# Kernel optimization log

Measured on AMD Instinct MI355X. Metric: run time of the kernel, lower is better.

The kernel has to match this reference:

```python
import jax, jax.numpy as jnp
import numpy as np

N_NODES = 100000
N_EDGES = 600000
N_FEAT = 166
HID = 128


def _ln(x, g, b, eps=1e-5):
    m = x.mean(-1, keepdims=True)
    v = ((x - m) ** 2).mean(-1, keepdims=True)
    return (x - m) * jax.lax.rsqrt(v + eps) * g + b


def _gcn(h, row, col, em, W, b, n):
    # PyG GCNConv with add_self_loops=True; em is a 0/1 edge mask (recent/history split)
    hl = h @ W.T  # [N,H], PyG internal Linear has no bias
    deg = jax.ops.segment_sum(em, col, num_segments=n) + 1.0  # +1 for self loop
    dis = jax.lax.rsqrt(deg)
    coef = em * dis[row] * dis[col]
    agg = jax.ops.segment_sum(hl[row] * coef[:, None], col, num_segments=n)
    agg = agg + hl * (dis * dis)[:, None]  # self-loop message
    return agg + b


def setup_inputs():
    key = jax.random.key(0)
    ks = jax.random.split(key, 16)
    f32 = jnp.float32
    H = HID
    z = lambda *s: jnp.zeros(s, f32)
    nrm = lambda k, s, sc=0.05: jax.random.normal(k, s, f32) * sc
    return {
        "x": jax.random.normal(ks[0], (N_NODES, N_FEAT), f32),
        "edge_index": jax.random.randint(ks[1], (2, N_EDGES), 0, N_NODES, jnp.int32),
        "timestamps": jax.random.uniform(ks[2], (N_EDGES,), f32),
        "memory": nrm(ks[3], (N_NODES, H), 0.1),
        "W_in": nrm(ks[4], (H, N_FEAT)), "b_in": z(H),
        "W_time": nrm(ks[5], (H, 1)), "b_time": z(H),
        "W_ih": nrm(ks[6], (3 * H, H)), "W_hh": nrm(ks[7], (3 * H, H)),
        "b_ih": z(3 * H), "b_hh": z(3 * H),
        "W_gr": nrm(ks[8], (H, H)), "b_gr": z(H),
        "W_gh": nrm(ks[9], (H, H)), "b_gh": z(H),
        "ln_pa_g": jnp.ones((H,), f32), "ln_pa_b": z(H),
        "Wv": nrm(ks[10], (H, H)), "bv": z(H),
        "Wo": nrm(ks[11], (H, H)), "bo": z(H),
        "ln_at_g": jnp.ones((H,), f32), "ln_at_b": z(H),
        "W1": nrm(ks[12], (64, H)), "b1": z(64),
        "W2": nrm(ks[13], (2, 64)), "b2": z(2),
    }


def reference(x, edge_index, timestamps, memory, W_in, b_in, W_time, b_time,
              W_ih, W_hh, b_ih, b_hh, W_gr, b_gr, W_gh, b_gh,
              ln_pa_g, ln_pa_b, Wv, bv, Wo, bo, ln_at_g, ln_at_b,
              W1, b1, W2, b2):
    n = x.shape[0]
    row, col = edge_index[0], edge_index[1]
    # input projection + scatter-max temporal encoding
    h = x @ W_in.T + b_in
    nt = jnp.maximum(jax.ops.segment_max(timestamps, col, num_segments=n), 0.0)  # torch_scatter max inits at 0
    tmin, tmax = nt.min(), nt.max()
    nt = jnp.where(tmax > tmin, (nt - tmin) / (tmax - tmin + 1e-8), nt)
    h = h + nt[:, None] * W_time[:, 0] + b_time  # Linear(1, H)
    h = jax.nn.relu(h)
    h = h + memory
    # gather -> GRUCell -> scatter memory update for nodes touched by any edge
    upd = jnp.zeros((n,), bool).at[edge_index.reshape(-1)].set(True)
    gi = h @ W_ih.T + b_ih
    gh = memory @ W_hh.T + b_hh
    ir, iz, ic = jnp.split(gi, 3, axis=1)
    hr, hz, hc = jnp.split(gh, 3, axis=1)
    r = jax.nn.sigmoid(ir + hr)
    z = jax.nn.sigmoid(iz + hz)
    c = jnp.tanh(ic + r * hc)
    new_memory = jnp.where(upd[:, None], (1.0 - z) * c + z * memory, memory)
    # split edges by median timestamp, two GCN paths
    med = jnp.median(timestamps)
    m_rec = (timestamps >= med).astype(h.dtype)
    h_rec = _gcn(h, row, col, m_rec, W_gr, b_gr, n)
    h_his = _gcn(h, row, col, 1.0 - m_rec, W_gh, b_gh, n)
    # multi-path aggregation with softmax over per-path mean scores
    stacked = jnp.stack([h_rec, h_his], axis=1)  # [N,2,H]
    w = jax.nn.softmax(stacked.mean(-1), axis=-1)[..., None]
    h = _ln((stacked * w).sum(1), ln_pa_g, ln_pa_b)
    # anomaly attention: L=S=1 per "batch" element, so softmax over one key == 1
    # => attended = out_proj(v_proj(x)); query path cancels exactly
    attended = (h @ Wv.T + bv) @ Wo.T + bo
    h = _ln(h + attended, ln_at_g, ln_at_b)
    # classifier (eval mode: dropout = identity)
    logits = jax.nn.relu(h @ W1.T + b1) @ W2.T + b2
    return logits, new_memory
```

## Files before the change

### kernel.cpp

```cpp
#include <hip/hip_runtime.h>

#define NN 100000
#define NE 600000
#define NF 166
#define NH 128
#define NNH 12800000

enum { EPI_PLAIN = 0, EPI_RELU = 2, EPI_H = 3, EPI_HEAD = 4 };

typedef short bf16x8 __attribute__((ext_vector_type(8)));
typedef float f32x16 __attribute__((ext_vector_type(16)));

__device__ __forceinline__ unsigned short f2bf(float f) {
  unsigned u = __float_as_uint(f);
  u += 0x7fffu + ((u >> 16) & 1u);
  return (unsigned short)(u >> 16);
}

__device__ __forceinline__ void gl_lds16(const void* g, void* l) {
  __builtin_amdgcn_global_load_lds((__attribute__((address_space(1))) void*)(void*)g,
                                   (__attribute__((address_space(3))) void*)l, 16, 0, 0);
}

template<int EPI, bool WF32, bool WB16, bool BIAS2, bool CONC, bool DUALA, int NT>
__launch_bounds__(256)
__global__ void mgemm(const unsigned short* __restrict__ A, int lda,
                      const unsigned short* __restrict__ A2,
                      const unsigned short* __restrict__ W, int ldw,
                      float* __restrict__ C, int ldc,
                      unsigned short* __restrict__ Cb, int ldcb,
                      int K, int M,
                      const float* __restrict__ bias, const float* __restrict__ bias2,
                      const float* __restrict__ wtv, const float* __restrict__ ntv,
                      const float* __restrict__ mem, const int* __restrict__ scal)
{
  __shared__ unsigned short As[128 * 64];
  __shared__ unsigned short Bs[128 * 64];
  const int tid = threadIdx.x;
  const int wave = tid >> 6, lane = tid & 63;
  const int row0 = blockIdx.y * 128, col0 = blockIdx.x * 128;
  if (DUALA && blockIdx.x) { A = A2; bias = bias2; }
  const int hi = lane >> 5, l5 = lane & 31, l3 = lane & 7;
  f32x16 acc[NT] = {};

  for (int k0 = 0; k0 < K; k0 += 64) {
    const unsigned short* Asrc = A;
    int kk = k0;
    if (CONC && k0 >= 128) { Asrc = A2; kk = k0 - 128; }
    __syncthreads();
#pragma unroll
    for (int q = 0; q < 4; ++q) {
      int id = q * 256 + tid;
      int r = id >> 3, cch = id & 7;
      int sw = ((cch ^ (r & 7)) << 3);
      int gr = row0 + r; if (gr > NN - 1) gr = NN - 1;
      gl_lds16(Asrc + (size_t)gr * lda + kk + sw, &As[(q * 256 + wave * 64) * 8]);
      if (q < NT) {
        int gm = col0 + r; if (gm > M - 1) gm = M - 1;
        gl_lds16(W + (size_t)gm * ldw + k0 + sw, &Bs[(q * 256 + wave * 64) * 8]);
      }
    }
    __syncthreads();
#pragma unroll
    for (int s = 0; s < 4; ++s) {
      int slot8 = (((s * 2 + hi) ^ l3) << 3);
      bf16x8 a = *(const bf16x8*)&As[(wave * 32 + l5) * 64 + slot8];
#pragma unroll
      for (int t = 0; t < NT; ++t) {
        bf16x8 b = *(const bf16x8*)&Bs[(t * 32 + l5) * 64 + slot8];
        acc[t] = __builtin_amdgcn_mfma_f32_32x32x16_bf16(a, b, acc[t], 0, 0, 0);
      }
    }
  }

  float tmin = 0.f, tmax = 0.f;
  if (EPI == EPI_H) { tmin = __int_as_float(scal[5]); tmax = __int_as_float(scal[6]); }
  float bc[NT], wc[NT];
#pragma unroll
  for (int t = 0; t < NT; ++t) {
    int gcol = col0 + t * 32 + l5;
    int bcol = DUALA ? (gcol & 127) : gcol;
    bc[t] = bias ? bias[bcol] : 0.f;
    if (BIAS2) bc[t] += bias2[gcol];
    if (EPI == EPI_H) { bc[t] += bias2[gcol]; wc[t] = wtv[gcol]; }
  }
#pragma unroll
  for (int rg = 0; rg < 16; ++rg) {
    int lr = (rg & 3) + 8 * (rg >> 2) + 4 * hi;
    int grow = row0 + wave * 32 + lr;
    if (grow >= NN) continue;
    float ntn = 0.f;
    if (EPI == EPI_H) {
      ntn = ntv[grow];
      if (tmax > tmin) ntn = (ntn - tmin) / (tmax - tmin + 1e-8f);
    }
    float hv[NT];
#pragma unroll
    for (int t = 0; t < NT; ++t) {
      float v = acc[t][rg] + bc[t];
      if (EPI == EPI_RELU || EPI == EPI_HEAD) v = fmaxf(v, 0.f);
      if (EPI == EPI_H) {
        v += ntn * wc[t];
        v = fmaxf(v, 0.f);
        v += mem[(size_t)grow * NH + (col0 + t * 32 + l5)];
      }
      hv[t] = v;
    }
    if (EPI == EPI_HEAD) {
      float p0 = hv[0] * wtv[l5]      + hv[1] * wtv[32 + l5];
      float p1 = hv[0] * wtv[64 + l5] + hv[1] * wtv[96 + l5];
#pragma unroll
      for (int d = 1; d < 32; d <<= 1) { p0 += __shfl_xor(p0, d); p1 += __shfl_xor(p1, d); }
      if (l5 == 0) {
        C[(size_t)grow * 2]     = p0 + bias2[0];
        C[(size_t)grow * 2 + 1] = p1 + bias2[1];
      }
    } else {
#pragma unroll
      for (int t = 0; t < NT; ++t) {
        int gcol = col0 + t * 32 + l5;
        if (WF32) C[(size_t)grow * ldc + gcol] = hv[t];
        if (WB16) Cb[(size_t)grow * ldcb + gcol] = f2bf(hv[t]);
      }
    }
  }
}

__global__ void conv_x(const float* __restrict__ x, unsigned short* __restrict__ xb)
{
  int i = blockIdx.x * 256 + threadIdx.x;
  if (i >= NN * 192) return;
  int n = i / 192, c = i - n * 192;
  xb[i] = (c < NF) ? f2bf(x[n * NF + c]) : (unsigned short)0;
}

__global__ void conv_mem(const float* __restrict__ m, unsigned short* __restrict__ mb)
{
  int i = blockIdx.x * 256 + threadIdx.x;
  if (i >= NNH) return;
  mb[i] = f2bf(m[i]);
}

__global__ void conv_w(const float* __restrict__ Wi, const float* __restrict__ Wih,
                       const float* __restrict__ Whh, const float* __restrict__ Wgr,
                       const float* __restrict__ Wgh, const float* __restrict__ Wv,
                       const float* __restrict__ Wo, const float* __restrict__ W1,
                       unsigned short* __restrict__ wb)
{
  int i = blockIdx.x * 256 + threadIdx.x;
  if (i >= 196608) return;
  float v;
  if (i < 24576)       { int r = i / 192, c = i - r * 192; v = (c < NF) ? Wi[r * NF + c] : 0.f; }
  else if (i < 90112)  { int j = i - 24576; int r = j >> 8, c = j & 255;
                         v = (c < 128) ? Wih[r * 128 + c] : Whh[r * 128 + (c - 128)]; }
  else if (i < 122880) { int j = i - 90112; int r = j >> 7, c = j & 127;
                         v = (r < 128) ? Wih[(256 + r) * 128 + c] : Whh[(128 + r) * 128 + c]; }
  else if (i < 139264) v = Wgr[i - 122880];
  else if (i < 155648) v = Wgh[i - 139264];
  else if (i < 172032) v = Wv[i - 155648];
  else if (i < 188416) v = Wo[i - 172032];
  else                 v = W1[i - 188416];
  wb[i] = f2bf(v);
}

__global__ void compose_att(const float* __restrict__ Wv, const float* __restrict__ Wo,
                            const float* __restrict__ bv, const float* __restrict__ bo,
                            unsigned short* __restrict__ wout, float* __restrict__ bout)
{
  int i = blockIdx.x * 256 + threadIdx.x;
  if (i >= 16384) return;
  int r = i >> 7, c = i & 127;
  float s = 0.f;
  for (int k = 0; k < 128; ++k) s = fmaf(Wo[r * 128 + k], Wv[k * 128 + c], s);
  wout[i] = f2bf(s);
  if (c == 0) {
    float t = bo[r];
    for (int k = 0; k < 128; ++k) t = fmaf(Wo[r * 128 + k], bv[k], t);
    bout[r] = t;
  }
}

__device__ __forceinline__ int ts_bin(float t) {
  int b = (int)(t * 65536.0f);
  return b > 65535 ? 65535 : (b < 0 ? 0 : b);
}

__global__ void edge_pass1(const int* __restrict__ row, const int* __restrict__ col,
                           const float* __restrict__ ts,
                           float* nt, int* upd, int* cnt_all, int* hist1)
{
  int e = blockIdx.x * 256 + threadIdx.x;
  if (e >= NE) return;
  int r = row[e], c = col[e];
  float t = ts[e];
  atomicMax((int*)(nt + c), __float_as_int(t));
  upd[r] = 1; upd[c] = 1;
  atomicAdd(cnt_all + c, 1);
  atomicAdd(hist1 + ts_bin(t), 1);
}

__global__ void node_minmax(const float* __restrict__ nt, int* scal)
{
  int i = blockIdx.x * 256 + threadIdx.x;
  float v = (i < NN) ? nt[i] : nt[0];
  float vmin = v, vmax = v;
#pragma unroll
  for (int d = 1; d < 64; d <<= 1) {
    vmin = fminf(vmin, __shfl_xor(vmin, d));
    vmax = fmaxf(vmax, __shfl_xor(vmax, d));
  }
  __shared__ float smin[4], smax[4];
  int lane = threadIdx.x & 63, w = threadIdx.x >> 6;
  if (lane == 0) { smin[w] = vmin; smax[w] = vmax; }
  __syncthreads();
  if (threadIdx.x == 0) {
    float a = fminf(fminf(smin[0], smin[1]), fminf(smin[2], smin[3]));
    float b = fmaxf(fmaxf(smax[0], smax[1]), fmaxf(smax[2], smax[3]));
    atomicMin(scal + 5, __float_as_int(a));
    atomicMax(scal + 6, __float_as_int(b));
  }
}

__global__ void scan_hist1(const int* __restrict__ hist, int* scal)
{
  const int K1 = 299999, K2 = 300000;
  __shared__ int sums[256];
  __shared__ int pre[257];
  int t = threadIdx.x;
  int s = 0;
  for (int i = 0; i < 256; ++i) s += hist[t * 256 + i];
  sums[t] = s;
  __syncthreads();
  if (t == 0) { int run = 0; for (int i = 0; i < 256; ++i) { pre[i] = run; run += sums[i]; } pre[256] = run; }
  __syncthreads();
  int base = pre[t], nexts = base + sums[t];
  if (K1 >= base && K1 < nexts) {
    int run = base;
    for (int i = 0; i < 256; ++i) {
      int cv = hist[t * 256 + i];
      if (K1 < run + cv) { scal[0] = t * 256 + i; scal[1] = run; break; }
      run += cv;
    }
  }
  if (K2 >= base && K2 < nexts) {
    int run = base;
    for (int i = 0; i < 256; ++i) {
      int cv = hist[t * 256 + i];
      if (K2 < run + cv) { scal[2] = t * 256 + i; scal[3] = run; break; }
      run += cv;
    }
  }
}

#define CAND_CAP 4096
__global__ void collect_cand(const float* __restrict__ ts, const int* __restrict__ scal,
                             float* cand1, float* cand2, int* ccnt)
{
  int e = blockIdx.x * 256 + threadIdx.x;
  if (e >= NE) return;
  float t = ts[e];
  int b = ts_bin(t);
  if (b == scal[0]) {
    int s = atomicAdd(ccnt + 0, 1);
    if (s < CAND_CAP) cand1[s] = t;
  }
  if (b == scal[2]) {
    int s = atomicAdd(ccnt + 1, 1);
    if (s < CAND_CAP) cand2[s] = t;
  }
}

__global__ void select_med(const float* __restrict__ c1, const float* __restrict__ c2,
                           const int* __restrict__ ccnt, int* scal)
{
  __shared__ float res[2];
  for (int which = 0; which < 2; ++which) {
    const float* c = which ? c2 : c1;
    int m = ccnt[which]; if (m > CAND_CAP) m = CAND_CAP;
    int rank = which ? (300000 - scal[3]) : (299999 - scal[1]);
    for (int i = threadIdx.x; i < m; i += 256) {
      float v = c[i];
      int less = 0, eq = 0;
      for (int j = 0; j < m; ++j) { float w = c[j]; less += (w < v); eq += (w == v); }
      if (less <= rank && rank < less + eq) res[which] = v;
    }
  }
  __syncthreads();
  if (threadIdx.x == 0)
    ((float*)scal)[4] = 0.5f * (res[0] + res[1]);
}

__global__ void csr_scan1(const int* __restrict__ cnt, int* loc, int* bsum)
{
  __shared__ int s[256];
  int t = threadIdx.x;
  int i = blockIdx.x * 256 + t;
  int v = (i < NN) ? cnt[i] : 0;
  s[t] = v;
  __syncthreads();
  for (int d = 1; d < 256; d <<= 1) {
    int add = (t >= d) ? s[t - d] : 0;
    __syncthreads();
    s[t] += add;
    __syncthreads();
  }
  if (i < NN) loc[i] = s[t] - v;
  if (t == 255) bsum[blockIdx.x] = s[255];
}

__global__ void csr_scan2(int* bsum, int nb)
{
  if (threadIdx.x == 0) {
    int run = 0;
    for (int i = 0; i < nb; ++i) { int v = bsum[i]; bsum[i] = run; run += v; }
  }
}

__global__ void csr_scan3(const int* __restrict__ loc, const int* __restrict__ bsum,
                          int* off, int* fillpos)
{
  int i = blockIdx.x * 256 + threadIdx.x;
  if (i < NN) {
    int o = loc[i] + bsum[i >> 8];
    off[i] = o;
    fillpos[i] = o;
  }
  if (i == 0) off[NN] = NE;
}

__global__ void csr_fill(const int* __restrict__ row, const int* __restrict__ col,
                         const float* __restrict__ ts, const int* __restrict__ scal,
                         int* fillpos, int* elist, int* cnt_rec)
{
  int e = blockIdx.x * 256 + threadIdx.x;
  if (e >= NE) return;
  int c = col[e], r = row[e];
  int rec = (ts[e] >= __int_as_float(scal[4])) ? 1 : 0;
  if (rec) atomicAdd(cnt_rec + c, 1);
  int slot = atomicAdd(fillpos + c, 1);
  elist[slot] = r | (rec << 31);
}

__global__ void node_dis(const int* __restrict__ cnt_all, const int* __restrict__ cnt_rec,
                         float* dr, float* dh)
{
  int n = blockIdx.x * 256 + threadIdx.x;
  if (n >= NN) return;
  int ca = cnt_all[n], cr = cnt_rec[n];
  dr[n] = rsqrtf((float)cr + 1.f);
  dh[n] = rsqrtf((float)(ca - cr) + 1.f);
}

__device__ __forceinline__ float gru1(float rp, float zp, float ic, float hc, float mv) {
  float r = 1.f / (1.f + expf(-rp));
  float z = 1.f / (1.f + expf(-zp));
  float c = tanhf(ic + r * hc);
  return (1.f - z) * c + z * mv;
}

__global__ void gru_kernel(const float* __restrict__ RZ, const float* __restrict__ ICHC,
                           const float* __restrict__ mem, const int* __restrict__ upd,
                           float* __restrict__ out)
{
  int idx = blockIdx.x * 256 + threadIdx.x;
  if (idx >= NN * 32) return;
  int n = idx >> 5, q = (idx & 31) << 2;
  size_t p128 = (size_t)n * 128 + q;
  size_t p256 = (size_t)n * 256 + q;
  float4 mv = *(const float4*)(mem + p128);
  float4 o = mv;
  if (upd[n]) {
    float4 rp = *(const float4*)(RZ + p256);
    float4 zp = *(const float4*)(RZ + p256 + 128);
    float4 ic = *(const float4*)(ICHC + p256);
    float4 hc = *(const float4*)(ICHC + p256 + 128);
    o.x = gru1(rp.x, zp.x, ic.x, hc.x, mv.x);
    o.y = gru1(rp.y, zp.y, ic.y, hc.y, mv.y);
    o.z = gru1(rp.z, zp.z, ic.z, hc.z, mv.z);
    o.w = gru1(rp.w, zp.w, ic.w, hc.w, mv.w);
  }
  *(float4*)(out + p128) = o;
}

__global__ void gather_combine(const int* __restrict__ off, const int* __restrict__ elist,
                               const float* __restrict__ dis_r, const float* __restrict__ dis_h,
                               const float* __restrict__ hl2,
                               const float* __restrict__ bgr, const float* __restrict__ bgh,
                               const float* __restrict__ g, const float* __restrict__ b,
                               float* h2f, unsigned short* h2b)
{
  int n = blockIdx.x * 4 + (threadIdx.x >> 6);
  if (n >= NN) return;
  int lane = threadIdx.x & 63;
  int o0 = off[n], o1 = off[n + 1];
  float dnr = dis_r[n], dnh = dis_h[n];
  float arx = 0.f, ary = 0.f, ahx = 0.f, ahy = 0.f;
  int j = o0;
  for (; j + 1 < o1; j += 2) {
    int p0 = elist[j], p1 = elist[j + 1];
    int r0 = p0 & 0x7fffffff, r1 = p1 & 0x7fffffff;
    int c0 = ((unsigned)p0) >> 31, c1 = ((unsigned)p1) >> 31;
    float d0 = c0 ? dis_r[r0] : dis_h[r0];
    float d1 = c1 ? dis_r[r1] : dis_h[r1];
    const float2 v0 = *(const float2*)(hl2 + (size_t)r0 * 256 + ((c0 ^ 1) << 7) + (lane << 1));
    const float2 v1 = *(const float2*)(hl2 + (size_t)r1 * 256 + ((c1 ^ 1) << 7) + (lane << 1));
    float k0 = d0 * (c0 ? dnr : dnh);
    float k1 = d1 * (c1 ? dnr : dnh);
    if (c0) { arx = fmaf(k0, v0.x, arx); ary = fmaf(k0, v0.y, ary); }
    else    { ahx = fmaf(k0, v0.x, ahx); ahy = fmaf(k0, v0.y, ahy); }
    if (c1) { arx = fmaf(k1, v1.x, arx); ary = fmaf(k1, v1.y, ary); }
    else    { ahx = fmaf(k1, v1.x, ahx); ahy = fmaf(k1, v1.y, ahy); }
  }
  if (j < o1) {
    int p0 = elist[j];
    int r0 = p0 & 0x7fffffff;
    int c0 = ((unsigned)p0) >> 31;
    float d0 = c0 ? dis_r[r0] : dis_h[r0];
    const float2 v0 = *(const float2*)(hl2 + (size_t)r0 * 256 + ((c0 ^ 1) << 7) + (lane << 1));
    float k0 = d0 * (c0 ? dnr : dnh);
    if (c0) { arx = fmaf(k0, v0.x, arx); ary = fmaf(k0, v0.y, ary); }
    else    { ahx = fmaf(k0, v0.x, ahx); ahy = fmaf(k0, v0.y, ahy); }
  }
  const float2 lr = *(const float2*)(hl2 + (size_t)n * 256 + (lane << 1));
  const float2 lh = *(const float2*)(hl2 + (size_t)n * 256 + 128 + (lane << 1));
  float2 br = *(const float2*)(bgr + (lane << 1));
  float2 bh = *(const float2*)(bgh + (lane << 1));
  float rx = arx + lr.x * dnr * dnr + br.x;
  float ry = ary + lr.y * dnr * dnr + br.y;
  float hx = ahx + lh.x * dnh * dnh + bh.x;
  float hy = ahy + lh.y * dnh * dnh + bh.y;
  float sa = rx + ry, sc = hx + hy;
#pragma unroll
  for (int d = 1; d < 64; d <<= 1) { sa += __shfl_xor(sa, d); sc += __shfl_xor(sc, d); }
  float m0 = sa * (1.f / 128.f), m1 = sc * (1.f / 128.f);
  float mx = fmaxf(m0, m1);
  float e0 = expf(m0 - mx), e1 = expf(m1 - mx);
  float inv = 1.f / (e0 + e1);
  float w0 = e0 * inv, w1 = e1 * inv;
  float yx = w0 * rx + w1 * hx;
  float yy = w0 * ry + w1 * hy;
  float s = yx + yy;
#pragma unroll
  for (int d = 1; d < 64; d <<= 1) s += __shfl_xor(s, d);
  float mean = s * (1.f / 128.f);
  float dx = yx - mean, dy = yy - mean;
  float vv = dx * dx + dy * dy;
#pragma unroll
  for (int d = 1; d < 64; d <<= 1) vv += __shfl_xor(vv, d);
  float rstd = rsqrtf(vv * (1.f / 128.f) + 1e-5f);
  float2 gg = *(const float2*)(g + (lane << 1));
  float2 bb = *(const float2*)(b + (lane << 1));
  float ox = dx * rstd * gg.x + bb.x;
  float oy = dy * rstd * gg.y + bb.y;
  int offo = n * NH + (lane << 1);
  *(float2*)(h2f + offo) = make_float2(ox, oy);
  *(unsigned*)(h2b + offo) = (unsigned)f2bf(ox) | ((unsigned)f2bf(oy) << 16);
}

__global__ void ln_residual(const float* __restrict__ x, const float* __restrict__ y,
                            const float* __restrict__ g, const float* __restrict__ b,
                            unsigned short* out)
{
  int n = blockIdx.x * 4 + (threadIdx.x >> 6);
  if (n >= NN) return;
  int lane = threadIdx.x & 63;
  int off = n * NH + (lane << 1);
  float2 xv = *(const float2*)(x + off);
  float2 yv = *(const float2*)(y + off);
  float ax = xv.x + yv.x, ay = xv.y + yv.y;
  float s = ax + ay;
#pragma unroll
  for (int d = 1; d < 64; d <<= 1) s += __shfl_xor(s, d);
  float mean = s * (1.f / 128.f);
  float dx = ax - mean, dy = ay - mean;
  float vv = dx * dx + dy * dy;
#pragma unroll
  for (int d = 1; d < 64; d <<= 1) vv += __shfl_xor(vv, d);
  float rstd = rsqrtf(vv * (1.f / 128.f) + 1e-5f);
  float2 gg = *(const float2*)(g + (lane << 1));
  float2 bb = *(const float2*)(b + (lane << 1));
  float ox = dx * rstd * gg.x + bb.x;
  float oy = dy * rstd * gg.y + bb.y;
  *(unsigned*)(out + off) = (unsigned)f2bf(ox) | ((unsigned)f2bf(oy) << 16);
}

extern "C" void kernel_launch(void* const* d_in, const int* in_sizes, int n_in,
                              void* d_out, int out_size, void* d_ws, size_t ws_size,
                              hipStream_t stream)
{
  const float* x      = (const float*)d_in[0];
  const int*   ei     = (const int*)  d_in[1];
  const float* ts     = (const float*)d_in[2];
  const float* mem    = (const float*)d_in[3];
  const float* W_in   = (const float*)d_in[4];
  const float* b_in   = (const float*)d_in[5];
  const float* W_time = (const float*)d_in[6];
  const float* b_time = (const float*)d_in[7];
  const float* W_ih   = (const float*)d_in[8];
  const float* W_hh   = (const float*)d_in[9];
  const float* b_ih   = (const float*)d_in[10];
  const float* b_hh   = (const float*)d_in[11];
  const float* W_gr   = (const float*)d_in[12];
  const float* b_gr   = (const float*)d_in[13];
  const float* W_gh   = (const float*)d_in[14];
  const float* b_gh   = (const float*)d_in[15];
  const float* ln_pa_g= (const float*)d_in[16];
  const float* ln_pa_b= (const float*)d_in[17];
  const float* Wv     = (const float*)d_in[18];
  const float* bv     = (const float*)d_in[19];
  const float* Wo     = (const float*)d_in[20];
  const float* bo     = (const float*)d_in[21];
  const float* ln_at_g= (const float*)d_in[22];
  const float* ln_at_b= (const float*)d_in[23];
  const float* W1     = (const float*)d_in[24];
  const float* b1     = (const float*)d_in[25];
  const float* W2     = (const float*)d_in[26];
  const float* b2     = (const float*)d_in[27];

  const int* row = ei;
  const int* col = ei + NE;
  float* out_logits = (float*)d_out;
  float* out_mem    = (float*)d_out + NN * 2;

  float* ws = (float*)d_ws;
  unsigned short* hb  = (unsigned short*)(ws);
  float* rz           = ws + 6400000;
  unsigned short* xb  = (unsigned short*)(ws + 6400000);
  int* hist1          = (int*)(ws + 16000000);
  float* ichc         = ws + 32000000;
  unsigned short* memb= (unsigned short*)(ws + 57600000);
  unsigned short* wb  = (unsigned short*)(ws + 64000000);
  float* nt           = ws + 64100000;
  float* dis_r        = ws + 64200000;
  float* dis_h        = ws + 64300000;
  int* cnt_all        = (int*)(ws + 64400000);
  int* cnt_rec        = (int*)(ws + 64500000);
  int* upd            = (int*)(ws + 64600000);
  int* scal           = (int*)(ws + 64700000);
  float* batt         = ws + 64705000;
  float* cand1        = ws + 64710000;
  float* cand2        = ws + 64715000;
  int* ccnt           = (int*)(ws + 64720000);
  float* h2f   = ws + 6400000;
  int* off     = (int*)(ws + 19200000);
  int* fillpos = (int*)(ws + 19350000);
  int* loc     = (int*)(ws + 19500000);
  int* bsum    = (int*)(ws + 19700000);
  int* elist   = (int*)(ws + 19800000);
  float* hl2   = ws + 32000000;
  unsigned short* h2bb = hb;
  float* att           = ws + 32000000;
  unsigned short* rb   = (unsigned short*)(ws + 44800000);

  unsigned short* wb_in = wb;
  unsigned short* wb_rz = wb + 24576;
  unsigned short* wb_c  = wb + 90112;
  unsigned short* wb_gr = wb + 122880;
  unsigned short* wb_v  = wb + 155648;
  unsigned short* wb_o  = wb + 172032;
  unsigned short* wb_1  = wb + 188416;

  hipMemsetAsync(nt,      0, NN * 4, stream);
  hipMemsetAsync(cnt_all, 0, NN * 4, stream);
  hipMemsetAsync(cnt_rec, 0, NN * 4, stream);
  hipMemsetAsync(upd,     0, NN * 4, stream);
  hipMemsetAsync(hist1,   0, 65536 * 4, stream);
  hipMemsetAsync(scal,    0, 16 * 4, stream);
  hipMemsetAsync(scal + 5,0x7f, 4, stream);
  hipMemsetAsync(ccnt,    0, 8, stream);

  const int eb  = (NE + 255) / 256;
  const int nb  = (NN + 255) / 256;
  dim3 blk(256);

  edge_pass1  <<<eb, 256, 0, stream>>>(row, col, ts, nt, upd, cnt_all, hist1);
  node_minmax <<<nb, 256, 0, stream>>>(nt, scal);
  scan_hist1  <<<1, 256, 0, stream>>>(hist1, scal);
  collect_cand<<<eb, 256, 0, stream>>>(ts, scal, cand1, cand2, ccnt);
  select_med  <<<1, 256, 0, stream>>>(cand1, cand2, ccnt, scal);

  conv_w     <<<768, 256, 0, stream>>>(W_in, W_ih, W_hh, W_gr, W_gh, Wv, Wo, W1, wb);
  compose_att<<<64, 256, 0, stream>>>(Wv, Wo, bv, bo, wb_o, batt);
  conv_x     <<<75000, 256, 0, stream>>>(x, xb);
  conv_mem   <<<50000, 256, 0, stream>>>(mem, memb);

  auto gg = [](int M) { return dim3((unsigned)((M + 127) / 128), (NN + 127) / 128); };

  mgemm<EPI_H, false, true, false, false, false, 4><<<gg(128), blk, 0, stream>>>(
      xb, 192, nullptr, wb_in, 192, nullptr, 0, hb, NH, 192, 128,
      b_in, b_time, W_time, nt, mem, scal);
  mgemm<EPI_PLAIN, true, false, true, true, false, 4><<<gg(256), blk, 0, stream>>>(
      hb, NH, memb, wb_rz, 256, rz, 256, nullptr, 0, 256, 256,
      b_ih, b_hh, nullptr, nullptr, nullptr, nullptr);
  mgemm<EPI_PLAIN, true, false, false, false, true, 4><<<gg(256), blk, 0, stream>>>(
      hb, NH, memb, wb_c, NH, ichc, 256, nullptr, 0, 128, 256,
      b_ih + 256, b_hh + 256, nullptr, nullptr, nullptr, nullptr);
  gru_kernel<<<(NN * 32) / 256, 256, 0, stream>>>(rz, ichc, mem, upd, out_mem);

  csr_scan1<<<nb, 256, 0, stream>>>(cnt_all, loc, bsum);
  csr_scan2<<<1, 64, 0, stream>>>(bsum, nb);
  csr_scan3<<<nb, 256, 0, stream>>>(loc, bsum, off, fillpos);
  csr_fill <<<eb, 256, 0, stream>>>(row, col, ts, scal, fillpos, elist, cnt_rec);
  node_dis <<<nb, 256, 0, stream>>>(cnt_all, cnt_rec, dis_r, dis_h);

  mgemm<EPI_PLAIN, true, false, false, false, false, 4><<<gg(256), blk, 0, stream>>>(
      hb, NH, nullptr, wb_gr, NH, hl2, 256, nullptr, 0, 128, 256,
      nullptr, nullptr, nullptr, nullptr, nullptr, nullptr);

  gather_combine<<<(NN + 3) / 4, 256, 0, stream>>>(off, elist, dis_r, dis_h, hl2,
      b_gr, b_gh, ln_pa_g, ln_pa_b, h2f, h2bb);

  mgemm<EPI_PLAIN, true, false, false, false, false, 4><<<gg(128), blk, 0, stream>>>(
      h2bb, NH, nullptr, wb_o, NH, att, NH, nullptr, 0, 128, 128,
      batt, nullptr, nullptr, nullptr, nullptr, nullptr);
  ln_residual<<<(NN + 3) / 4, 256, 0, stream>>>(h2f, att, ln_at_g, ln_at_b, rb);

  mgemm<EPI_HEAD, false, false, false, false, false, 2><<<gg(64), blk, 0, stream>>>(
      rb, NH, nullptr, wb_1, NH, out_logits, 0, nullptr, 0, 128, 64,
      b1, b2, W2, nullptr, nullptr, nullptr);

  (void)in_sizes; (void)n_in; (void)out_size; (void)ws_size;
}
```

Baseline: 811.7 us.

## Fuse LN into attention GEMM, drop conv_mem, and store intermediates in fp16

The attention output projection now runs LayerNorm and the residual add in its epilogue, which removes the separate ln_residual kernel and the fp32 att and h2f round trips. The input-projection GEMM writes the bf16 copy of memory as a side output, so the conv_mem pass is gone. GRU pre-activations, GCN linear outputs and h2 are stored as fp16 rather than fp32, which halves gather and GRU traffic. Wider N tiles (NT=8) let one block cover all 256 output columns. The attention GEMM now uses the fp16 MFMA, and the change accepts fp16 rounding on these intermediates.

Result: faster. 758.2 us (-6.6%).

```diff
diff --git a/kernel.cpp b/kernel.cpp
--- a/kernel.cpp
+++ b/kernel.cpp
@@ -6,10 +6,13 @@
 #define NH 128
 #define NNH 12800000
 
-enum { EPI_PLAIN = 0, EPI_RELU = 2, EPI_H = 3, EPI_HEAD = 4 };
+enum { EPI_PLAIN = 0, EPI_RELU = 2, EPI_H = 3, EPI_HEAD = 4, EPI_ATTLN = 5 };
 
 typedef short bf16x8 __attribute__((ext_vector_type(8)));
 typedef float f32x16 __attribute__((ext_vector_type(16)));
+typedef _Float16 f16x2 __attribute__((ext_vector_type(2)));
+typedef _Float16 f16x4 __attribute__((ext_vector_type(4)));
+typedef _Float16 f16x8 __attribute__((ext_vector_type(8)));
 
 __device__ __forceinline__ unsigned short f2bf(float f) {
   unsigned u = __float_as_uint(f);
@@ -17,12 +20,16 @@
   return (unsigned short)(u >> 16);
 }
 
+__device__ __forceinline__ unsigned short f2h(float f) {
+  return __builtin_bit_cast(unsigned short, (_Float16)f);
+}
+
 __device__ __forceinline__ void gl_lds16(const void* g, void* l) {
   __builtin_amdgcn_global_load_lds((__attribute__((address_space(1))) void*)(void*)g,
                                    (__attribute__((address_space(3))) void*)l, 16, 0, 0);
 }
 
-template<int EPI, bool WF32, bool WB16, bool BIAS2, bool CONC, bool DUALA, int NT>
+template<int EPI, int OUTK, bool BIAS2, bool CONC, bool DUALA, bool F16, int NT>
 __launch_bounds__(256)
 __global__ void mgemm(const unsigned short* __restrict__ A, int lda,
                       const unsigned short* __restrict__ A2,
@@ -35,10 +42,10 @@
                       const float* __restrict__ mem, const int* __restrict__ scal)
 {
   __shared__ unsigned short As[128 * 64];
-  __shared__ unsigned short Bs[128 * 64];
+  __shared__ unsigned short Bs[NT * 32 * 64];
   const int tid = threadIdx.x;
   const int wave = tid >> 6, lane = tid & 63;
-  const int row0 = blockIdx.y * 128, col0 = blockIdx.x * 128;
+  const int row0 = blockIdx.y * 128, col0 = blockIdx.x * NT * 32;
   if (DUALA && blockIdx.x) { A = A2; bias = bias2; }
   const int hi = lane >> 5, l5 = lane & 31, l3 = lane & 7;
   f32x16 acc[NT] = {};
@@ -55,10 +62,14 @@
       int sw = ((cch ^ (r & 7)) << 3);
       int gr = row0 + r; if (gr > NN - 1) gr = NN - 1;
       gl_lds16(Asrc + (size_t)gr * lda + kk + sw, &As[(q * 256 + wave * 64) * 8]);
-      if (q < NT) {
-        int gm = col0 + r; if (gm > M - 1) gm = M - 1;
-        gl_lds16(W + (size_t)gm * ldw + k0 + sw, &Bs[(q * 256 + wave * 64) * 8]);
-      }
+    }
+#pragma unroll
+    for (int q = 0; q < NT; ++q) {
+      int id = q * 256 + tid;
+      int r = id >> 3, cch = id & 7;
+      int sw = ((cch ^ (r & 7)) << 3);
+      int gm = col0 + r; if (gm > M - 1) gm = M - 1;
+      gl_lds16(W + (size_t)gm * ldw + k0 + sw, &Bs[(q * 256 + wave * 64) * 8]);
     }
     __syncthreads();
 #pragma unroll
@@ -68,21 +79,26 @@
 #pragma unroll
       for (int t = 0; t < NT; ++t) {
         bf16x8 b = *(const bf16x8*)&Bs[(t * 32 + l5) * 64 + slot8];
-        acc[t] = __builtin_amdgcn_mfma_f32_32x32x16_bf16(a, b, acc[t], 0, 0, 0);
+        if (F16)
+          acc[t] = __builtin_amdgcn_mfma_f32_32x32x16_f16(
+              __builtin_bit_cast(f16x8, a), __builtin_bit_cast(f16x8, b), acc[t], 0, 0, 0);
+        else
+          acc[t] = __builtin_amdgcn_mfma_f32_32x32x16_bf16(a, b, acc[t], 0, 0, 0);
       }
     }
   }
 
   float tmin = 0.f, tmax = 0.f;
   if (EPI == EPI_H) { tmin = __int_as_float(scal[5]); tmax = __int_as_float(scal[6]); }
-  float bc[NT], wc[NT];
+  float bc[NT], wc[NT], b2c[NT];
 #pragma unroll
   for (int t = 0; t < NT; ++t) {
     int gcol = col0 + t * 32 + l5;
     int bcol = DUALA ? (gcol & 127) : gcol;
     bc[t] = bias ? bias[bcol] : 0.f;
     if (BIAS2) bc[t] += bias2[gcol];
-    if (EPI == EPI_H) { bc[t] += bias2[gcol]; wc[t] = wtv[gcol]; }
+    if (EPI == EPI_H)     { bc[t] += bias2[gcol]; wc[t] = wtv[gcol]; }
+    if (EPI == EPI_ATTLN) { wc[t] = wtv[gcol]; b2c[t] = bias2[gcol]; }
   }
 #pragma unroll
   for (int rg = 0; rg < 16; ++rg) {
@@ -102,9 +118,31 @@
       if (EPI == EPI_H) {
         v += ntn * wc[t];
         v = fmaxf(v, 0.f);
-        v += mem[(size_t)grow * NH + (col0 + t * 32 + l5)];
+        float mv = mem[(size_t)grow * NH + (col0 + t * 32 + l5)];
+        v += mv;
+        ((unsigned short*)C)[(size_t)grow * NH + (col0 + t * 32 + l5)] = f2bf(mv);
       }
       hv[t] = v;
+    }
+    if (EPI == EPI_ATTLN) {
+      const _Float16* h2r = (const _Float16*)mem;
+      float s = 0.f;
+#pragma unroll
+      for (int t = 0; t < NT; ++t) {
+        hv[t] += (float)h2r[(size_t)grow * NH + (col0 + t * 32 + l5)];
+        s += hv[t];
+      }
+#pragma unroll
+      for (int d = 1; d < 32; d <<= 1) s += __shfl_xor(s, d);
+      float mean = s * (1.f / 128.f);
+      float var = 0.f;
+#pragma unroll
+      for (int t = 0; t < NT; ++t) { hv[t] -= mean; var += hv[t] * hv[t]; }
+#pragma unroll
+      for (int d = 1; d < 32; d <<= 1) var += __shfl_xor(var, d);
+      float rstd = rsqrtf(var * (1.f / 128.f) + 1e-5f);
+#pragma unroll
+      for (int t = 0; t < NT; ++t) hv[t] = hv[t] * rstd * wc[t] + b2c[t];
     }
     if (EPI == EPI_HEAD) {
       float p0 = hv[0] * wtv[l5]      + hv[1] * wtv[32 + l5];
@@ -119,8 +157,9 @@
 #pragma unroll
       for (int t = 0; t < NT; ++t) {
         int gcol = col0 + t * 32 + l5;
-        if (WF32) C[(size_t)grow * ldc + gcol] = hv[t];
-        if (WB16) Cb[(size_t)grow * ldcb + gcol] = f2bf(hv[t]);
+        if (OUTK == 1) C[(size_t)grow * ldc + gcol] = hv[t];
+        if (OUTK == 2) Cb[(size_t)grow * ldcb + gcol] = f2bf(hv[t]);
+        if (OUTK == 3) Cb[(size_t)grow * ldcb + gcol] = f2h(hv[t]);
       }
     }
   }
@@ -132,13 +171,6 @@
   if (i >= NN * 192) return;
   int n = i / 192, c = i - n * 192;
   xb[i] = (c < NF) ? f2bf(x[n * NF + c]) : (unsigned short)0;
-}
-
-__global__ void conv_mem(const float* __restrict__ m, unsigned short* __restrict__ mb)
-{
-  int i = blockIdx.x * 256 + threadIdx.x;
-  if (i >= NNH) return;
-  mb[i] = f2bf(m[i]);
 }
 
 __global__ void conv_w(const float* __restrict__ Wi, const float* __restrict__ Wih,
@@ -165,14 +197,14 @@
 
 __global__ void compose_att(const float* __restrict__ Wv, const float* __restrict__ Wo,
                             const float* __restrict__ bv, const float* __restrict__ bo,
-                            unsigned short* __restrict__ wout, float* __restrict__ bout)
+                            _Float16* __restrict__ wout, float* __restrict__ bout)
 {
   int i = blockIdx.x * 256 + threadIdx.x;
   if (i >= 16384) return;
   int r = i >> 7, c = i & 127;
   float s = 0.f;
   for (int k = 0; k < 128; ++k) s = fmaf(Wo[r * 128 + k], Wv[k * 128 + c], s);
-  wout[i] = f2bf(s);
+  wout[i] = (_Float16)s;
   if (c == 0) {
     float t = bo[r];
     for (int k = 0; k < 128; ++k) t = fmaf(Wo[r * 128 + k], bv[k], t);
@@ -358,7 +390,7 @@
   return (1.f - z) * c + z * mv;
 }
 
-__global__ void gru_kernel(const float* __restrict__ RZ, const float* __restrict__ ICHC,
+__global__ void gru_kernel(const _Float16* __restrict__ RZ, const _Float16* __restrict__ ICHC,
                            const float* __restrict__ mem, const int* __restrict__ upd,
                            float* __restrict__ out)
 {
@@ -370,65 +402,67 @@
   float4 mv = *(const float4*)(mem + p128);
   float4 o = mv;
   if (upd[n]) {
-    float4 rp = *(const float4*)(RZ + p256);
-    float4 zp = *(const float4*)(RZ + p256 + 128);
-    float4 ic = *(const float4*)(ICHC + p256);
-    float4 hc = *(const float4*)(ICHC + p256 + 128);
-    o.x = gru1(rp.x, zp.x, ic.x, hc.x, mv.x);
-    o.y = gru1(rp.y, zp.y, ic.y, hc.y, mv.y);
-    o.z = gru1(rp.z, zp.z, ic.z, hc.z, mv.z);
-    o.w = gru1(rp.w, zp.w, ic.w, hc.w, mv.w);
+    f16x4 rp = *(const f16x4*)(RZ + p256);
+    f16x4 zp = *(const f16x4*)(RZ + p256 + 128);
+    f16x4 ic = *(const f16x4*)(ICHC + p256);
+    f16x4 hc = *(const f16x4*)(ICHC + p256 + 128);
+    o.x = gru1((float)rp[0], (float)zp[0], (float)ic[0], (float)hc[0], mv.x);
+    o.y = gru1((float)rp[1], (float)zp[1], (float)ic[1], (float)hc[1], mv.y);
+    o.z = gru1((float)rp[2], (float)zp[2], (float)ic[2], (float)hc[2], mv.z);
+    o.w = gru1((float)rp[3], (float)zp[3], (float)ic[3], (float)hc[3], mv.w);
   }
   *(float4*)(out + p128) = o;
 }
 
 __global__ void gather_combine(const int* __restrict__ off, const int* __restrict__ elist,
                                const float* __restrict__ dis_r, const float* __restrict__ dis_h,
-                               const float* __restrict__ hl2,
+                               const _Float16* __restrict__ hl2,
                                const float* __restrict__ bgr, const float* __restrict__ bgh,
                                const float* __restrict__ g, const float* __restrict__ b,
-                               float* h2f, unsigned short* h2b)
+                               _Float16* __restrict__ h2)
 {
   int n = blockIdx.x * 4 + (threadIdx.x >> 6);
   if (n >= NN) return;
   int lane = threadIdx.x & 63;
-  int o0 = off[n], o1 = off[n + 1];
+  int o0 = __builtin_amdgcn_readfirstlane(off[n]);
+  int o1 = __builtin_amdgcn_readfirstlane(off[n + 1]);
   float dnr = dis_r[n], dnh = dis_h[n];
   float arx = 0.f, ary = 0.f, ahx = 0.f, ahy = 0.f;
   int j = o0;
   for (; j + 1 < o1; j += 2) {
-    int p0 = elist[j], p1 = elist[j + 1];
+    int p0 = __builtin_amdgcn_readfirstlane(elist[j]);
+    int p1 = __builtin_amdgcn_readfirstlane(elist[j + 1]);
     int r0 = p0 & 0x7fffffff, r1 = p1 & 0x7fffffff;
     int c0 = ((unsigned)p0) >> 31, c1 = ((unsigned)p1) >> 31;
     float d0 = c0 ? dis_r[r0] : dis_h[r0];
     float d1 = c1 ? dis_r[r1] : dis_h[r1];
-    const float2 v0 = *(const float2*)(hl2 + (size_t)r0 * 256 + ((c0 ^ 1) << 7) + (lane << 1));
-    const float2 v1 = *(const float2*)(hl2 + (size_t)r1 * 256 + ((c1 ^ 1) << 7) + (lane << 1));
+    f16x2 v0 = *(const f16x2*)(hl2 + (size_t)r0 * 256 + ((c0 ^ 1) << 7) + (lane << 1));
+    f16x2 v1 = *(const f16x2*)(hl2 + (size_t)r1 * 256 + ((c1 ^ 1) << 7) + (lane << 1));
     float k0 = d0 * (c0 ? dnr : dnh);
     float k1 = d1 * (c1 ? dnr : dnh);
-    if (c0) { arx = fmaf(k0, v0.x, arx); ary = fmaf(k0, v0.y, ary); }
-    else    { ahx = fmaf(k0, v0.x, ahx); ahy = fmaf(k0, v0.y, ahy); }
-    if (c1) { arx = fmaf(k1, v1.x, arx); ary = fmaf(k1, v1.y, ary); }
-    else    { ahx = fmaf(k1, v1.x, ahx); ahy = fmaf(k1, v1.y, ahy); }
+    if (c0) { arx = fmaf(k0, (float)v0[0], arx); ary = fmaf(k0, (float)v0[1], ary); }
+    else    { ahx = fmaf(k0, (float)v0[0], ahx); ahy = fmaf(k0, (float)v0[1], ahy); }
+    if (c1) { arx = fmaf(k1, (float)v1[0], arx); ary = fmaf(k1, (float)v1[1], ary); }
+    else    { ahx = fmaf(k1, (float)v1[0], ahx); ahy = fmaf(k1, (float)v1[1], ahy); }
   }
   if (j < o1) {
-    int p0 = elist[j];
+    int p0 = __builtin_amdgcn_readfirstlane(elist[j]);
     int r0 = p0 & 0x7fffffff;
     int c0 = ((unsigned)p0) >> 31;
     float d0 = c0 ? dis_r[r0] : dis_h[r0];
-    const float2 v0 = *(const float2*)(hl2 + (size_t)r0 * 256 + ((c0 ^ 1) << 7) + (lane << 1));
+    f16x2 v0 = *(const f16x2*)(hl2 + (size_t)r0 * 256 + ((c0 ^ 1) << 7) + (lane << 1));
     float k0 = d0 * (c0 ? dnr : dnh);
-    if (c0) { arx = fmaf(k0, v0.x, arx); ary = fmaf(k0, v0.y, ary); }
-    else    { ahx = fmaf(k0, v0.x, ahx); ahy = fmaf(k0, v0.y, ahy); }
-  }
-  const float2 lr = *(const float2*)(hl2 + (size_t)n * 256 + (lane << 1));
-  const float2 lh = *(const float2*)(hl2 + (size_t)n * 256 + 128 + (lane << 1));
+    if (c0) { arx = fmaf(k0, (float)v0[0], arx); ary = fmaf(k0, (float)v0[1], ary); }
+    else    { ahx = fmaf(k0, (float)v0[0], ahx); ahy = fmaf(k0, (float)v0[1], ahy); }
+  }
+  f16x2 lr = *(const f16x2*)(hl2 + (size_t)n * 256 + (lane << 1));
+  f16x2 lh = *(const f16x2*)(hl2 + (size_t)n * 256 + 128 + (lane << 1));
   float2 br = *(const float2*)(bgr + (lane << 1));
   float2 bh = *(const float2*)(bgh + (lane << 1));
-  float rx = arx + lr.x * dnr * dnr + br.x;
-  float ry = ary + lr.y * dnr * dnr + br.y;
-  float hx = ahx + lh.x * dnh * dnh + bh.x;
-  float hy = ahy + lh.y * dnh * dnh + bh.y;
+  float rx = arx + (float)lr[0] * dnr * dnr + br.x;
+  float ry = ary + (float)lr[1] * dnr * dnr + br.y;
+  float hx = ahx + (float)lh[0] * dnh * dnh + bh.x;
+  float hy = ahy + (float)lh[1] * dnh * dnh + bh.y;
   float sa = rx + ry, sc = hx + hy;
 #pragma unroll
   for (int d = 1; d < 64; d <<= 1) { sa += __shfl_xor(sa, d); sc += __shfl_xor(sc, d); }
@@ -450,38 +484,10 @@
   float rstd = rsqrtf(vv * (1.f / 128.f) + 1e-5f);
   float2 gg = *(const float2*)(g + (lane << 1));
   float2 bb = *(const float2*)(b + (lane << 1));
-  float ox = dx * rstd * gg.x + bb.x;
-  float oy = dy * rstd * gg.y + bb.y;
-  int offo = n * NH + (lane << 1);
-  *(float2*)(h2f + offo) = make_float2(ox, oy);
-  *(unsigned*)(h2b + offo) = (unsigned)f2bf(ox) | ((unsigned)f2bf(oy) << 16);
-}
-
-__global__ void ln_residual(const float* __restrict__ x, const float* __restrict__ y,
-                            const float* __restrict__ g, const float* __restrict__ b,
-                            unsigned short* out)
-{
-  int n = blockIdx.x * 4 + (threadIdx.x >> 6);
-  if (n >= NN) return;
-  int lane = threadIdx.x & 63;
-  int off = n * NH + (lane << 1);
-  float2 xv = *(const float2*)(x + off);
-  float2 yv = *(const float2*)(y + off);
-  float ax = xv.x + yv.x, ay = xv.y + yv.y;
-  float s = ax + ay;
-#pragma unroll
-  for (int d = 1; d < 64; d <<= 1) s += __shfl_xor(s, d);
-  float mean = s * (1.f / 128.f);
-  float dx = ax - mean, dy = ay - mean;
-  float vv = dx * dx + dy * dy;
-#pragma unroll
-  for (int d = 1; d < 64; d <<= 1) vv += __shfl_xor(vv, d);
-  float rstd = rsqrtf(vv * (1.f / 128.f) + 1e-5f);
-  float2 gg = *(const float2*)(g + (lane << 1));
-  float2 bb = *(const float2*)(b + (lane << 1));
-  float ox = dx * rstd * gg.x + bb.x;
-  float oy = dy * rstd * gg.y + bb.y;
-  *(unsigned*)(out + off) = (unsigned)f2bf(ox) | ((unsigned)f2bf(oy) << 16);
+  f16x2 o;
+  o[0] = (_Float16)(dx * rstd * gg.x + bb.x);
+  o[1] = (_Float16)(dy * rstd * gg.y + bb.y);
+  *(f16x2*)(h2 + (size_t)n * NH + (lane << 1)) = o;
 }
 
 extern "C" void kernel_launch(void* const* d_in, const int* in_sizes, int n_in,
@@ -523,40 +529,37 @@
   float* out_mem    = (float*)d_out + NN * 2;
 
   float* ws = (float*)d_ws;
-  unsigned short* hb  = (unsigned short*)(ws);
-  float* rz           = ws + 6400000;
-  unsigned short* xb  = (unsigned short*)(ws + 6400000);
-  int* hist1          = (int*)(ws + 16000000);
-  float* ichc         = ws + 32000000;
-  unsigned short* memb= (unsigned short*)(ws + 57600000);
-  unsigned short* wb  = (unsigned short*)(ws + 64000000);
-  float* nt           = ws + 64100000;
-  float* dis_r        = ws + 64200000;
-  float* dis_h        = ws + 64300000;
-  int* cnt_all        = (int*)(ws + 64400000);
-  int* cnt_rec        = (int*)(ws + 64500000);
-  int* upd            = (int*)(ws + 64600000);
-  int* scal           = (int*)(ws + 64700000);
-  float* batt         = ws + 64705000;
-  float* cand1        = ws + 64710000;
-  float* cand2        = ws + 64715000;
-  int* ccnt           = (int*)(ws + 64720000);
-  float* h2f   = ws + 6400000;
-  int* off     = (int*)(ws + 19200000);
-  int* fillpos = (int*)(ws + 19350000);
-  int* loc     = (int*)(ws + 19500000);
-  int* bsum    = (int*)(ws + 19700000);
-  int* elist   = (int*)(ws + 19800000);
-  float* hl2   = ws + 32000000;
-  unsigned short* h2bb = hb;
-  float* att           = ws + 32000000;
-  unsigned short* rb   = (unsigned short*)(ws + 44800000);
+  unsigned short* hb   = (unsigned short*)(ws);
+  _Float16* h2         = (_Float16*)(ws);
+  unsigned short* xb   = (unsigned short*)(ws + 6400000);
+  _Float16* rz         = (_Float16*)(ws + 6400000);
+  unsigned short* rb   = (unsigned short*)(ws + 6400000);
+  _Float16* ichc       = (_Float16*)(ws + 19200000);
+  _Float16* hl2        = (_Float16*)(ws + 32000000);
+  unsigned short* memb = (unsigned short*)(ws + 44800000);
+  unsigned short* wb   = (unsigned short*)(ws + 51200000);
+  float* nt            = ws + 51350000;
+  float* dis_r         = ws + 51450000;
+  float* dis_h         = ws + 51550000;
+  int* cnt_all         = (int*)(ws + 51650000);
+  int* cnt_rec         = (int*)(ws + 51750000);
+  int* upd             = (int*)(ws + 51850000);
+  int* scal            = (int*)(ws + 51950000);
+  float* batt          = ws + 51960000;
+  float* cand1         = ws + 51970000;
+  float* cand2         = ws + 51980000;
+  int* ccnt            = (int*)(ws + 51990000);
+  int* hist1           = (int*)(ws + 52000000);
+  int* off             = (int*)(ws + 52100000);
+  int* fillpos         = (int*)(ws + 52250000);
+  int* loc             = (int*)(ws + 52400000);
+  int* bsum            = (int*)(ws + 52550000);
+  int* elist           = (int*)(ws + 52600000);
 
   unsigned short* wb_in = wb;
   unsigned short* wb_rz = wb + 24576;
   unsigned short* wb_c  = wb + 90112;
   unsigned short* wb_gr = wb + 122880;
-  unsigned short* wb_v  = wb + 155648;
   unsigned short* wb_o  = wb + 172032;
   unsigned short* wb_1  = wb + 188416;
 
@@ -572,6 +575,7 @@
   const int eb  = (NE + 255) / 256;
   const int nb  = (NN + 255) / 256;
   dim3 blk(256);
+  const unsigned gy = (NN + 127) / 128;
 
   edge_pass1  <<<eb, 256, 0, stream>>>(row, col, ts, nt, upd, cnt_all, hist1);
   node_minmax <<<nb, 256, 0, stream>>>(nt, scal);
@@ -580,20 +584,17 @@
   select_med  <<<1, 256, 0, stream>>>(cand1, cand2, ccnt, scal);
 
   conv_w     <<<768, 256, 0, stream>>>(W_in, W_ih, W_hh, W_gr, W_gh, Wv, Wo, W1, wb);
-  compose_att<<<64, 256, 0, stream>>>(Wv, Wo, bv, bo, wb_o, batt);
+  compose_att<<<64, 256, 0, stream>>>(Wv, Wo, bv, bo, (_Float16*)wb_o, batt);
   conv_x     <<<75000, 256, 0, stream>>>(x, xb);
-  conv_mem   <<<50000, 256, 0, stream>>>(mem, memb);
-
-  auto gg = [](int M) { return dim3((unsigned)((M + 127) / 128), (NN + 127) / 128); };
-
-  mgemm<EPI_H, false, true, false, false, false, 4><<<gg(128), blk, 0, stream>>>(
-      xb, 192, nullptr, wb_in, 192, nullptr, 0, hb, NH, 192, 128,
+
+  mgemm<EPI_H, 2, false, false, false, false, 4><<<dim3(1, gy), blk, 0, stream>>>(
+      xb, 192, nullptr, wb_in, 192, (float*)memb, 0, hb, NH, 192, 128,
       b_in, b_time, W_time, nt, mem, scal);
-  mgemm<EPI_PLAIN, true, false, true, true, false, 4><<<gg(256), blk, 0, stream>>>(
-      hb, NH, memb, wb_rz, 256, rz, 256, nullptr, 0, 256, 256,
+  mgemm<EPI_PLAIN, 3, true, true, false, false, 8><<<dim3(1, gy), blk, 0, stream>>>(
+      hb, NH, memb, wb_rz, 256, nullptr, 0, (unsigned short*)rz, 256, 256, 256,
       b_ih, b_hh, nullptr, nullptr, nullptr, nullptr);
-  mgemm<EPI_PLAIN, true, false, false, false, true, 4><<<gg(256), blk, 0, stream>>>(
-      hb, NH, memb, wb_c, NH, ichc, 256, nullptr, 0, 128, 256,
+  mgemm<EPI_PLAIN, 3, false, false, true, false, 4><<<dim3(2, gy), blk, 0, stream>>>(
+      hb, NH, memb, wb_c, NH, nullptr, 0, (unsigned short*)ichc, 256, 128, 256,
       b_ih + 256, b_hh + 256, nullptr, nullptr, nullptr, nullptr);
   gru_kernel<<<(NN * 32) / 256, 256, 0, stream>>>(rz, ichc, mem, upd, out_mem);
 
@@ -603,19 +604,18 @@
   csr_fill <<<eb, 256, 0, stream>>>(row, col, ts, scal, fillpos, elist, cnt_rec);
   node_dis <<<nb, 256, 0, stream>>>(cnt_all, cnt_rec, dis_r, dis_h);
 
-  mgemm<EPI_PLAIN, true, false, false, false, false, 4><<<gg(256), blk, 0, stream>>>(
-      hb, NH, nullptr, wb_gr, NH, hl2, 256, nullptr, 0, 128, 256,
+  mgemm<EPI_PLAIN, 3, false, false, false, false, 8><<<dim3(1, gy), blk, 0, stream>>>(
+      hb, NH, nullptr, wb_gr, NH, nullptr, 0, (unsigned short*)hl2, 256, 128, 256,
       nullptr, nullptr, nullptr, nullptr, nullptr, nullptr);
 
   gather_combine<<<(NN + 3) / 4, 256, 0, stream>>>(off, elist, dis_r, dis_h, hl2,
-      b_gr, b_gh, ln_pa_g, ln_pa_b, h2f, h2bb);
-
-  mgemm<EPI_PLAIN, true, false, false, false, false, 4><<<gg(128), blk, 0, stream>>>(
-      h2bb, NH, nullptr, wb_o, NH, att, NH, nullptr, 0, 128, 128,
-      batt, nullptr, nullptr, nullptr, nullptr, nullptr);
-  ln_residual<<<(NN + 3) / 4, 256, 0, stream>>>(h2f, att, ln_at_g, ln_at_b, rb);
-
-  mgemm<EPI_HEAD, false, false, false, false, false, 2><<<gg(64), blk, 0, stream>>>(
+      b_gr, b_gh, ln_pa_g, ln_pa_b, h2);
+
+  mgemm<EPI_ATTLN, 2, false, false, false, true, 4><<<dim3(1, gy), blk, 0, stream>>>(
+      (const unsigned short*)h2, NH, nullptr, wb_o, NH, nullptr, 0, rb, NH, 128, 128,
+      batt, ln_at_b, ln_at_g, nullptr, (const float*)h2, scal);
+
+  mgemm<EPI_HEAD, 0, false, false, false, false, 2><<<dim3(1, gy), blk, 0, stream>>>(
       rb, NH, nullptr, wb_1, NH, out_logits, 0, nullptr, 0, 128, 64,
       b1, b2, W2, nullptr, nullptr, nullptr);
 
```
